# Optimization experiments

Hardware: AMD Instinct MI355X
Metric: run time of the kernel (lower is better)

## Reference

```python
import jax, jax.numpy as jnp
import numpy as np

B, D, H, W, Q = 16, 768, 64, 64, 128


def setup_inputs() -> dict:
    key = jax.random.key(0)
    ks = jax.random.split(key, 6)
    s = 0.02  # param init scale
    return {
        "visual_feat": jax.random.normal(ks[0], (B, D, H, W), jnp.float32),
        "text_feat": jax.random.normal(ks[1], (B, Q, D), jnp.float32),
        "Wq": jax.random.normal(ks[2], (D, D), jnp.float32) * s,
        "bq": jnp.zeros((D,), jnp.float32),
        "Wk": jax.random.normal(ks[3], (D, D), jnp.float32) * s,
        "bk": jnp.zeros((D,), jnp.float32),
        "Wv": jax.random.normal(ks[4], (D, D), jnp.float32) * s,
        "bv": jnp.zeros((D,), jnp.float32),
    }


def _entropy_weights(x):
    # x: [B, T, D] -> softmax over features, per-token entropy, softmax over tokens -> [B, T]
    p = jax.nn.softmax(x, axis=-1)
    ent = -jnp.sum(p * jnp.log(p + 1e-9), axis=-1)
    return jax.nn.softmax(ent, axis=-1)


def reference(visual_feat, text_feat, Wq, bq, Wk, bk, Wv, bv):
    b, d, h, w = visual_feat.shape
    vf = visual_feat.reshape(b, d, h * w).transpose(0, 2, 1)  # [B, N, D]
    ve = _entropy_weights(vf)          # [B, N]
    te = _entropy_weights(text_feat)   # [B, Q]
    q = vf @ Wq.T + bq                 # [B, N, D]
    k = text_feat @ Wk.T + bk          # [B, Q, D]
    v = text_feat @ Wv.T + bv          # [B, Q, D]
    attn = jnp.einsum('bnd,bqd->bnq', q, k) / jnp.sqrt(jnp.float32(d))
    attn = attn * (ve[:, :, None] * te[:, None, :])  # entropy outer-product modulation
    attn = jax.nn.softmax(attn, axis=-1)
    enhanced = jnp.einsum('bnq,bqd->bnd', attn, v)   # [B, N, D]
    return enhanced.transpose(0, 2, 1).reshape(b, d, h, w)
```

## Files before the change

kernel.cpp:

```cpp
#include <hip/hip_runtime.h>

#define B_ 16
#define D_ 768
#define N_ 4096
#define Q_ 128

typedef __attribute__((ext_vector_type(4))) float f32x4;
typedef __attribute__((ext_vector_type(8))) short short8;
typedef __attribute__((ext_vector_type(4))) short sv4;

__device__ __forceinline__ unsigned short f2bf(float f) {
  union { float f; unsigned u; } x; x.f = f;
  unsigned u = x.u;
  unsigned r = u + 0x7fffu + ((u >> 16) & 1u);
  return (unsigned short)(r >> 16);
}
__device__ __forceinline__ float bf2f(unsigned short h) {
  union { unsigned u; float f; } x; x.u = ((unsigned)h) << 16;
  return x.f;
}

__global__ __launch_bounds__(256) void prep_kernel(
    const float* __restrict__ Wk, const float* __restrict__ Wv,
    const float* __restrict__ Wq, const float* __restrict__ text,
    unsigned short* __restrict__ Wkb, unsigned short* __restrict__ Wvb,
    unsigned short* __restrict__ WqTb, unsigned short* __restrict__ textb,
    float* __restrict__ ent_t) {
  __shared__ float tile[32][33];
  const int z = blockIdx.z;
  const int t = threadIdx.x;
  if (z <= 1) {
    const float* src = z ? Wv : Wk;
    unsigned short* dst = z ? Wvb : Wkb;
    int i = (blockIdx.y * 24 + blockIdx.x) * 256 + t;
    float4 v = ((const float4*)src)[i];
    ushort4 o;
    o.x = f2bf(v.x); o.y = f2bf(v.y); o.z = f2bf(v.z); o.w = f2bf(v.w);
    ((ushort4*)dst)[i] = o;
  } else if (z == 2) {
    int bx = blockIdx.x * 32, by = blockIdx.y * 32;
    int tx = t & 31, ty = t >> 5;
    #pragma unroll
    for (int i = 0; i < 32; i += 8)
      tile[ty + i][tx] = Wq[(size_t)(by + ty + i) * D_ + bx + tx];
    __syncthreads();
    #pragma unroll
    for (int i = 0; i < 32; i += 8)
      WqTb[(size_t)(bx + ty + i) * D_ + by + tx] = f2bf(tile[tx][ty + i]);
  } else {
    int idx = blockIdx.y * 24 + blockIdx.x;
    if (idx >= 512) return;
    int row = idx * 4 + (t >> 6);
    int lane = t & 63;
    const float4* src = (const float4*)(text + (size_t)row * D_);
    ushort4* dst = (ushort4*)(textb + (size_t)row * D_);
    float s = 0.f, tt = 0.f;
    #pragma unroll
    for (int j = 0; j < 3; j++) {
      float4 v = src[lane + 64 * j];
      float e0 = __expf(v.x), e1 = __expf(v.y), e2 = __expf(v.z), e3 = __expf(v.w);
      s += (e0 + e1) + (e2 + e3);
      tt += v.x * e0 + v.y * e1;
      tt += v.z * e2 + v.w * e3;
      ushort4 o;
      o.x = f2bf(v.x); o.y = f2bf(v.y); o.z = f2bf(v.z); o.w = f2bf(v.w);
      dst[lane + 64 * j] = o;
    }
    #pragma unroll
    for (int off = 32; off; off >>= 1) {
      s += __shfl_xor(s, off);
      tt += __shfl_xor(tt, off);
    }
    if (lane == 0) ent_t[row] = __logf(s) - tt / s;
  }
}

__global__ __launch_bounds__(256) void gemm_kvT_kernel(
    const unsigned short* __restrict__ A, const unsigned short* __restrict__ Wkb,
    const float* __restrict__ bk, unsigned short* __restrict__ kb,
    const unsigned short* __restrict__ Wvb, const float* __restrict__ bv,
    unsigned short* __restrict__ vTb) {
  constexpr int LDA = 72;
  __shared__ unsigned short As[64 * LDA];
  __shared__ unsigned short Bs[64 * LDA];
  const bool isV = blockIdx.y >= 12;
  const unsigned short* Bm = isV ? Wvb : Wkb;
  const float* bias = isV ? bv : bk;
  unsigned short* C = isV ? vTb : kb;
  int m0 = blockIdx.x * 64, n0 = (isV ? blockIdx.y - 12 : blockIdx.y) * 64;
  int t = threadIdx.x, wave = t >> 6, lane = t & 63;
  int wm = (wave & 1) * 32, wn = (wave >> 1) * 32;
  int fl = lane & 15, fq = lane >> 4;
  f32x4 acc[2][2];
  #pragma unroll
  for (int i = 0; i < 2; i++)
    #pragma unroll
    for (int j = 0; j < 2; j++) acc[i][j] = {0.f, 0.f, 0.f, 0.f};
  for (int k0 = 0; k0 < D_; k0 += 64) {
    __syncthreads();
    #pragma unroll
    for (int i = 0; i < 2; i++) {
      int c = t + 256 * i;
      int sr = c >> 3, sc = (c & 7) * 8;
      *(uint4*)(As + sr * LDA + sc) = *(const uint4*)(A + (size_t)(m0 + sr) * D_ + k0 + sc);
      *(uint4*)(Bs + sr * LDA + sc) = *(const uint4*)(Bm + (size_t)(n0 + sr) * D_ + k0 + sc);
    }
    __syncthreads();
    #pragma unroll
    for (int ks = 0; ks < 2; ks++) {
      short8 afr[2], bfr[2];
      #pragma unroll
      for (int i = 0; i < 2; i++)
        afr[i] = *(const short8*)(As + (wm + i * 16 + fl) * LDA + ks * 32 + fq * 8);
      #pragma unroll
      for (int j = 0; j < 2; j++)
        bfr[j] = *(const short8*)(Bs + (wn + j * 16 + fl) * LDA + ks * 32 + fq * 8);
      #pragma unroll
      for (int i = 0; i < 2; i++)
        #pragma unroll
        for (int j = 0; j < 2; j++)
          acc[i][j] = __builtin_amdgcn_mfma_f32_16x16x32_bf16(afr[i], bfr[j], acc[i][j], 0, 0, 0);
    }
  }
  #pragma unroll
  for (int i = 0; i < 2; i++)
    #pragma unroll
    for (int j = 0; j < 2; j++) {
      int n = n0 + wn + j * 16 + fl;
      float bb = bias[n];
      #pragma unroll
      for (int r = 0; r < 4; r++) {
        int m = m0 + wm + i * 16 + fq * 4 + r;
        float val = acc[i][j][r] + bb;
        if (isV) {
          int bt = m >> 7, q = m & 127;
          C[((size_t)bt * D_ + n) * Q_ + q] = f2bf(val);
        } else {
          C[(size_t)m * D_ + n] = f2bf(val);
        }
      }
    }
}

__global__ __launch_bounds__(256) void gemm_kq_bias_kernel(
    const unsigned short* __restrict__ kb, const unsigned short* __restrict__ WqTb,
    unsigned short* __restrict__ kqb, const float* __restrict__ bq,
    float* __restrict__ skq) {
  constexpr int LDA = 72;
  __shared__ unsigned short As[64 * LDA];
  __shared__ unsigned short Bs[64 * LDA];
  const int t = threadIdx.x;
  if (blockIdx.y >= 12) {
    int idx = (blockIdx.y - 12) * 32 + blockIdx.x;
    int row = idx * 4 + (t >> 6);
    int lane = t & 63;
    const unsigned short* kr = kb + (size_t)row * D_;
    float s = 0.f;
    for (int k = lane; k < D_; k += 64) s += bq[k] * bf2f(kr[k]);
    #pragma unroll
    for (int off = 32; off; off >>= 1) s += __shfl_xor(s, off);
    if (lane == 0) skq[row] = s;
    return;
  }
  int m0 = blockIdx.x * 64, n0 = blockIdx.y * 64;
  int wave = t >> 6, lane = t & 63;
  int wm = (wave & 1) * 32, wn = (wave >> 1) * 32;
  int fl = lane & 15, fq = lane >> 4;
  f32x4 acc[2][2];
  #pragma unroll
  for (int i = 0; i < 2; i++)
    #pragma unroll
    for (int j = 0; j < 2; j++) acc[i][j] = {0.f, 0.f, 0.f, 0.f};
  for (int k0 = 0; k0 < D_; k0 += 64) {
    __syncthreads();
    #pragma unroll
    for (int i = 0; i < 2; i++) {
      int c = t + 256 * i;
      int sr = c >> 3, sc = (c & 7) * 8;
      *(uint4*)(As + sr * LDA + sc) = *(const uint4*)(kb + (size_t)(m0 + sr) * D_ + k0 + sc);
      *(uint4*)(Bs + sr * LDA + sc) = *(const uint4*)(WqTb + (size_t)(n0 + sr) * D_ + k0 + sc);
    }
    __syncthreads();
    #pragma unroll
    for (int ks = 0; ks < 2; ks++) {
      short8 afr[2], bfr[2];
      #pragma unroll
      for (int i = 0; i < 2; i++)
        afr[i] = *(const short8*)(As + (wm + i * 16 + fl) * LDA + ks * 32 + fq * 8);
      #pragma unroll
      for (int j = 0; j < 2; j++)
        bfr[j] = *(const short8*)(Bs + (wn + j * 16 + fl) * LDA + ks * 32 + fq * 8);
      #pragma unroll
      for (int i = 0; i < 2; i++)
        #pragma unroll
        for (int j = 0; j < 2; j++)
          acc[i][j] = __builtin_amdgcn_mfma_f32_16x16x32_bf16(afr[i], bfr[j], acc[i][j], 0, 0, 0);
    }
  }
  #pragma unroll
  for (int i = 0; i < 2; i++)
    #pragma unroll
    for (int j = 0; j < 2; j++) {
      int n = n0 + wn + j * 16 + fl;
      #pragma unroll
      for (int r = 0; r < 4; r++) {
        int m = m0 + wm + i * 16 + fq * 4 + r;
        kqb[(size_t)m * D_ + n] = f2bf(acc[i][j][r]);
      }
    }
}

__global__ __launch_bounds__(256, 2) void attn_s_kernel(
    const float* __restrict__ vis,
    const unsigned short* __restrict__ kq,
    float* __restrict__ S,
    float* __restrict__ ent_v)
{
  constexpr int LA = 68;
  constexpr int LB = 72;
  __shared__ unsigned short As[64 * LA];
  __shared__ unsigned short Bs[128 * LB];
  __shared__ float esh[512];

  const int bb = blockIdx.x >> 6;
  const int n0 = (blockIdx.x & 63) * 64;
  const int t = threadIdx.x;
  const int wave = t >> 6, lane = t & 63;
  const int fl = lane & 15, fq = lane >> 4;
  const int wm = (wave & 1) * 32;
  const int wq = (wave >> 1) * 64;

  const float* abase = vis + (size_t)bb * D_ * N_ + n0;
  const unsigned short* bbase = kq + (size_t)bb * Q_ * D_;

  f32x4 acc[2][4];
  #pragma unroll
  for (int i = 0; i < 2; i++)
    #pragma unroll
    for (int j = 0; j < 4; j++) acc[i][j] = {0.f, 0.f, 0.f, 0.f};

  const int smi = t & 63;
  const int ph = t >> 6;
  float es = 0.f, ets = 0.f;

  for (int k0 = 0; k0 < D_; k0 += 64) {
    __syncthreads();
    #pragma unroll
    for (int i = 0; i < 8; i++) {
      const int kk = 2 * (ph + 4 * i);
      const float v0 = abase[(size_t)(k0 + kk) * N_ + smi];
      const float v1 = abase[(size_t)(k0 + kk + 1) * N_ + smi];
      const float e0 = __expf(v0), e1 = __expf(v1);
      es += e0 + e1;
      ets += v0 * e0 + v1 * e1;
      const unsigned pk = (unsigned)f2bf(v0) | ((unsigned)f2bf(v1) << 16);
      *(unsigned*)(As + smi * LA + kk) = pk;
    }
    #pragma unroll
    for (int i = 0; i < 4; i++) {
      const int c = t + 256 * i;
      const int q = c >> 3, kc = (c & 7) * 8;
      const uint4 v = *(const uint4*)(bbase + (size_t)q * D_ + k0 + kc);
      *(uint4*)(Bs + q * LB + kc) = v;
    }
    __syncthreads();
    #pragma unroll
    for (int ks = 0; ks < 2; ks++) {
      short8 afr[2], bfr[4];
      #pragma unroll
      for (int i = 0; i < 2; i++) {
        const unsigned short* pa = As + (wm + i * 16 + fl) * LA + ks * 32 + fq * 8;
        sv4 lo = *(const sv4*)pa;
        sv4 hi = *(const sv4*)(pa + 4);
        afr[i] = __builtin_shufflevector(lo, hi, 0, 1, 2, 3, 4, 5, 6, 7);
      }
      #pragma unroll
      for (int j = 0; j < 4; j++)
        bfr[j] = *(const short8*)(Bs + (wq + j * 16 + fl) * LB + ks * 32 + fq * 8);
      #pragma unroll
      for (int i = 0; i < 2; i++)
        #pragma unroll
        for (int j = 0; j < 4; j++)
          acc[i][j] = __builtin_amdgcn_mfma_f32_16x16x32_bf16(afr[i], bfr[j], acc[i][j], 0, 0, 0);
    }
  }

  esh[t] = es;
  esh[256 + t] = ets;
  __syncthreads();
  if (t < 64) {
    const float Sx = esh[t] + esh[t + 64] + esh[t + 128] + esh[t + 192];
    const float Tx = esh[256 + t] + esh[320 + t] + esh[384 + t] + esh[448 + t];
    ent_v[(size_t)bb * N_ + n0 + t] = __logf(Sx) - Tx / Sx;
  }

  float* sbase = S + ((size_t)bb * N_ + n0) * Q_;
  #pragma unroll
  for (int i = 0; i < 2; i++)
    #pragma unroll
    for (int j = 0; j < 4; j++)
      #pragma unroll
      for (int r = 0; r < 4; r++)
        sbase[(size_t)(wm + i * 16 + fq * 4 + r) * Q_ + wq + j * 16 + fl] = acc[i][j][r];
}

__global__ __launch_bounds__(256, 2) void attn_pv_kernel(
    const float* __restrict__ S,
    const unsigned short* __restrict__ vT,
    const float* __restrict__ ent_v,
    const float* __restrict__ ent_t,
    const float* __restrict__ skq,
    float* __restrict__ out)
{
  constexpr int LP = 136;
  __shared__ unsigned short Ps[64 * LP];
  __shared__ unsigned short Vs[64 * LP];
  __shared__ float stats[2][64][2];
  __shared__ float tesh[128];
  __shared__ float vesh[64];
  __shared__ float zred[4];
  __shared__ float zsum, tsum;

  const int bb = blockIdx.x >> 6;
  const int n0 = (blockIdx.x & 63) * 64;
  const int t = threadIdx.x;
  const int wave = t >> 6, lane = t & 63;
  const int fl = lane & 15, fq = lane >> 4;
  const int wm = (wave & 1) * 32;
  const int wq = (wave >> 1) * 64;

  const float* evb = ent_v + (size_t)bb * N_;
  float zp = 0.f;
  #pragma unroll
  for (int i = 0; i < 16; i++) zp += __expf(evb[t + 256 * i]);
  #pragma unroll
  for (int off = 32; off; off >>= 1) zp += __shfl_xor(zp, off);
  if (lane == 0) zred[wave] = zp;
  if (t < 128) tesh[t] = __expf(ent_t[bb * 128 + t]);
  if (t < 64) vesh[t] = __expf(evb[n0 + t]);
  __syncthreads();
  if (t == 0) zsum = zred[0] + zred[1] + zred[2] + zred[3];
  if (t < 64) {
    float s = tesh[t] + tesh[t + 64];
    #pragma unroll
    for (int off = 32; off; off >>= 1) s += __shfl_xor(s, off);
    if (t == 0) tsum = s;
  }
  __syncthreads();
  const float rZ = 1.0f / zsum;
  const float rT = 1.0f / tsum;

  f32x4 acc[2][4];
  const float* sbase = S + ((size_t)bb * N_ + n0) * Q_;
  #pragma unroll
  for (int i = 0; i < 2; i++)
    #pragma unroll
    for (int j = 0; j < 4; j++)
      #pragma unroll
      for (int r = 0; r < 4; r++)
        acc[i][j][r] = sbase[(size_t)(wm + i * 16 + fq * 4 + r) * Q_ + wq + j * 16 + fl];

  const float rsD = 0.03608439182435161f;
  float tev[4], skv[4];
  #pragma unroll
  for (int j = 0; j < 4; j++) {
    int q = wq + j * 16 + fl;
    tev[j] = tesh[q] * rT;
    skv[j] = skq[bb * Q_ + q];
  }
  float vev4[2][4];
  #pragma unroll
  for (int i = 0; i < 2; i++)
    #pragma unroll
    for (int r = 0; r < 4; r++)
      vev4[i][r] = vesh[wm + i * 16 + fq * 4 + r] * rZ;

  float rmax[2][4], rsum[2][4];
  #pragma unroll
  for (int i = 0; i < 2; i++)
    #pragma unroll
    for (int r = 0; r < 4; r++) rmax[i][r] = -__builtin_inff();
  #pragma unroll
  for (int i = 0; i < 2; i++)
    #pragma unroll
    for (int j = 0; j < 4; j++)
      #pragma unroll
      for (int r = 0; r < 4; r++) {
        float L = (acc[i][j][r] + skv[j]) * rsD * vev4[i][r] * tev[j];
        acc[i][j][r] = L;
        rmax[i][r] = fmaxf(rmax[i][r], L);
      }
  #pragma unroll
  for (int off = 1; off < 16; off <<= 1)
    #pragma unroll
    for (int i = 0; i < 2; i++)
      #pragma unroll
      for (int r = 0; r < 4; r++)
        rmax[i][r] = fmaxf(rmax[i][r], __shfl_xor(rmax[i][r], off));
  #pragma unroll
  for (int i = 0; i < 2; i++)
    #pragma unroll
    for (int r = 0; r < 4; r++) rsum[i][r] = 0.f;
  #pragma unroll
  for (int i = 0; i < 2; i++)
    #pragma unroll
    for (int j = 0; j < 4; j++)
      #pragma unroll
      for (int r = 0; r < 4; r++) {
        float e = __expf(acc[i][j][r] - rmax[i][r]);
        acc[i][j][r] = e;
        rsum[i][r] += e;
      }
  #pragma unroll
  for (int off = 1; off < 16; off <<= 1)
    #pragma unroll
    for (int i = 0; i < 2; i++)
      #pragma unroll
      for (int r = 0; r < 4; r++) rsum[i][r] += __shfl_xor(rsum[i][r], off);

  const int qh = wq >> 6;
  if (fl == 0) {
    #pragma unroll
    for (int i = 0; i < 2; i++)
      #pragma unroll
      for (int r = 0; r < 4; r++) {
        int m = wm + i * 16 + fq * 4 + r;
        stats[qh][m][0] = rmax[i][r];
        stats[qh][m][1] = rsum[i][r];
      }
  }
  __syncthreads();
  float fac[2][4];
  #pragma unroll
  for (int i = 0; i < 2; i++)
    #pragma unroll
    for (int r = 0; r < 4; r++) {
      int m = wm + i * 16 + fq * 4 + r;
      float M2 = stats[1 - qh][m][0], S2 = stats[1 - qh][m][1];
      float Mf = fmaxf(rmax[i][r], M2);
      float sf = rsum[i][r] * __expf(rmax[i][r] - Mf) + S2 * __expf(M2 - Mf);
      fac[i][r] = __expf(rmax[i][r] - Mf) / sf;
    }
  #pragma unroll
  for (int i = 0; i < 2; i++)
    #pragma unroll
    for (int j = 0; j < 4; j++)
      #pragma unroll
      for (int r = 0; r < 4; r++) {
        int m = wm + i * 16 + fq * 4 + r;
        int q = wq + j * 16 + fl;
        Ps[m * LP + q] = f2bf(acc[i][j][r] * fac[i][r]);
      }

  const int wd = (wave & 1) * 32;
  const int wm2 = (wave >> 1) * 32;
  for (int dc = 0; dc < 12; dc++) {
    __syncthreads();
    const unsigned short* vbase = vT + ((size_t)bb * D_ + dc * 64) * Q_;
    #pragma unroll
    for (int i = 0; i < 4; i++) {
      const int c = t + 256 * i;
      const int d = c >> 4, qc = (c & 15) * 8;
      *(uint4*)(Vs + d * LP + qc) = *(const uint4*)(vbase + (size_t)d * Q_ + qc);
    }
    __syncthreads();
    f32x4 acc2[2][2];
    #pragma unroll
    for (int i = 0; i < 2; i++)
      #pragma unroll
      for (int j = 0; j < 2; j++) acc2[i][j] = {0.f, 0.f, 0.f, 0.f};
    #pragma unroll
    for (int ks = 0; ks < 4; ks++) {
      short8 vfr[2], pfr[2];
      #pragma unroll
      for (int i = 0; i < 2; i++)
        vfr[i] = *(const short8*)(Vs + (wd + i * 16 + fl) * LP + ks * 32 + fq * 8);
      #pragma unroll
      for (int j = 0; j < 2; j++)
        pfr[j] = *(const short8*)(Ps + (wm2 + j * 16 + fl) * LP + ks * 32 + fq * 8);
      #pragma unroll
      for (int i = 0; i < 2; i++)
        #pragma unroll
        for (int j = 0; j < 2; j++)
          acc2[i][j] = __builtin_amdgcn_mfma_f32_16x16x32_bf16(vfr[i], pfr[j], acc2[i][j], 0, 0, 0);
    }
    float* obase = out + ((size_t)bb * D_ + dc * 64) * N_ + n0;
    #pragma unroll
    for (int i = 0; i < 2; i++)
      #pragma unroll
      for (int j = 0; j < 2; j++) {
        int mm = wm2 + j * 16 + fl;
        #pragma unroll
        for (int r = 0; r < 4; r++) {
          int d = wd + i * 16 + fq * 4 + r;
          obase[(size_t)d * N_ + mm] = acc2[i][j][r];
        }
      }
  }
}

extern "C" void kernel_launch(void* const* d_in, const int* in_sizes, int n_in,
                              void* d_out, int out_size, void* d_ws, size_t ws_size,
                              hipStream_t stream) {
  const float* vis  = (const float*)d_in[0];
  const float* text = (const float*)d_in[1];
  const float* Wq   = (const float*)d_in[2];
  const float* bq   = (const float*)d_in[3];
  const float* Wk   = (const float*)d_in[4];
  const float* bk   = (const float*)d_in[5];
  const float* Wv   = (const float*)d_in[6];
  const float* bv   = (const float*)d_in[7];
  float* out = (float*)d_out;
  char* ws = (char*)d_ws;

  unsigned short* textb = (unsigned short*)(ws + 0);
  unsigned short* Wkb   = (unsigned short*)(ws + 3145728);
  unsigned short* Wvb   = (unsigned short*)(ws + 4325376);
  unsigned short* WqTb  = (unsigned short*)(ws + 5505024);
  unsigned short* kb    = (unsigned short*)(ws + 6684672);
  unsigned short* kqb   = (unsigned short*)(ws + 9830400);
  unsigned short* vTb   = (unsigned short*)(ws + 12976128);
  float* ent_t = (float*)(ws + 16121856);
  float* ent_v = (float*)(ws + 16138240);
  float* skq   = (float*)(ws + 16662528);
  float* Sbuf  = (float*)(ws + 16777216);

  prep_kernel<<<dim3(24, 24, 4), 256, 0, stream>>>(Wk, Wv, Wq, text,
                                                   Wkb, Wvb, WqTb, textb, ent_t);
  gemm_kvT_kernel<<<dim3(32, 24), 256, 0, stream>>>(textb, Wkb, bk, kb, Wvb, bv, vTb);
  gemm_kq_bias_kernel<<<dim3(32, 28), 256, 0, stream>>>(kb, WqTb, kqb, bq, skq);
  attn_s_kernel<<<1024, 256, 0, stream>>>(vis, kqb, Sbuf, ent_v);
  attn_pv_kernel<<<1024, 256, 0, stream>>>(Sbuf, vTb, ent_v, ent_t, skq, out);
}
```

Baseline: 430.7 us.

## Vectorize visual loads, store S in fragment layout, stage output through LDS

Measured after the change: 437.9 us. No clear change (+1.7%).

```diff
diff --git a/kernel.cpp b/kernel.cpp
--- a/kernel.cpp
+++ b/kernel.cpp
@@ -239,22 +239,23 @@
     #pragma unroll
     for (int j = 0; j < 4; j++) acc[i][j] = {0.f, 0.f, 0.f, 0.f};
 
-  const int smi = t & 63;
-  const int ph = t >> 6;
-  float es = 0.f, ets = 0.f;
+  const int col4 = t & 15;
+  float es4[4] = {0.f, 0.f, 0.f, 0.f}, ets4[4] = {0.f, 0.f, 0.f, 0.f};
 
   for (int k0 = 0; k0 < D_; k0 += 64) {
     __syncthreads();
     #pragma unroll
-    for (int i = 0; i < 8; i++) {
-      const int kk = 2 * (ph + 4 * i);
-      const float v0 = abase[(size_t)(k0 + kk) * N_ + smi];
-      const float v1 = abase[(size_t)(k0 + kk + 1) * N_ + smi];
-      const float e0 = __expf(v0), e1 = __expf(v1);
-      es += e0 + e1;
-      ets += v0 * e0 + v1 * e1;
-      const unsigned pk = (unsigned)f2bf(v0) | ((unsigned)f2bf(v1) << 16);
-      *(unsigned*)(As + smi * LA + kk) = pk;
+    for (int i = 0; i < 4; i++) {
+      const int row = (t >> 4) + 16 * i;
+      const float4 v = *(const float4*)(abase + (size_t)(k0 + row) * N_ + col4 * 4);
+      const float vv[4] = {v.x, v.y, v.z, v.w};
+      #pragma unroll
+      for (int j = 0; j < 4; j++) {
+        const float e = __expf(vv[j]);
+        es4[j] += e;
+        ets4[j] += vv[j] * e;
+        As[(col4 * 4 + j) * LA + row] = f2bf(vv[j]);
+      }
     }
     #pragma unroll
     for (int i = 0; i < 4; i++) {
@@ -285,23 +286,33 @@
     }
   }
 
-  esh[t] = es;
-  esh[256 + t] = ets;
+  #pragma unroll
+  for (int j = 0; j < 4; j++) {
+    es4[j] += __shfl_xor(es4[j], 16);
+    es4[j] += __shfl_xor(es4[j], 32);
+    ets4[j] += __shfl_xor(ets4[j], 16);
+    ets4[j] += __shfl_xor(ets4[j], 32);
+  }
+  if (lane < 16) {
+    #pragma unroll
+    for (int j = 0; j < 4; j++) {
+      esh[wave * 64 + lane * 4 + j] = es4[j];
+      esh[256 + wave * 64 + lane * 4 + j] = ets4[j];
+    }
+  }
   __syncthreads();
   if (t < 64) {
-    const float Sx = esh[t] + esh[t + 64] + esh[t + 128] + esh[t + 192];
+    const float Sx = esh[t] + esh[64 + t] + esh[128 + t] + esh[192 + t];
     const float Tx = esh[256 + t] + esh[320 + t] + esh[384 + t] + esh[448 + t];
     ent_v[(size_t)bb * N_ + n0 + t] = __logf(Sx) - Tx / Sx;
   }
 
-  float* sbase = S + ((size_t)bb * N_ + n0) * Q_;
+  float* sfrag = S + ((size_t)blockIdx.x * 256 + t) * 32;
   #pragma unroll
   for (int i = 0; i < 2; i++)
     #pragma unroll
     for (int j = 0; j < 4; j++)
-      #pragma unroll
-      for (int r = 0; r < 4; r++)
-        sbase[(size_t)(wm + i * 16 + fq * 4 + r) * Q_ + wq + j * 16 + fl] = acc[i][j][r];
+      *(f32x4*)(sfrag + (i * 4 + j) * 4) = acc[i][j];
 }
 
 __global__ __launch_bounds__(256, 2) void attn_pv_kernel(
@@ -313,6 +324,7 @@
     float* __restrict__ out)
 {
   constexpr int LP = 136;
+  constexpr int LN = 68;
   __shared__ unsigned short Ps[64 * LP];
   __shared__ unsigned short Vs[64 * LP];
   __shared__ float stats[2][64][2];
@@ -320,6 +332,7 @@
   __shared__ float vesh[64];
   __shared__ float zred[4];
   __shared__ float zsum, tsum;
+  float* Os = (float*)Vs;
 
   const int bb = blockIdx.x >> 6;
   const int n0 = (blockIdx.x & 63) * 64;
@@ -351,14 +364,12 @@
   const float rT = 1.0f / tsum;
 
   f32x4 acc[2][4];
-  const float* sbase = S + ((size_t)bb * N_ + n0) * Q_;
+  const float* sfrag = S + ((size_t)blockIdx.x * 256 + t) * 32;
   #pragma unroll
   for (int i = 0; i < 2; i++)
     #pragma unroll
     for (int j = 0; j < 4; j++)
-      #pragma unroll
-      for (int r = 0; r < 4; r++)
-        acc[i][j][r] = sbase[(size_t)(wm + i * 16 + fq * 4 + r) * Q_ + wq + j * 16 + fl];
+      acc[i][j] = *(const f32x4*)(sfrag + (i * 4 + j) * 4);
 
   const float rsD = 0.03608439182435161f;
   float tev[4], skv[4];
@@ -484,7 +495,7 @@
         for (int j = 0; j < 2; j++)
           acc2[i][j] = __builtin_amdgcn_mfma_f32_16x16x32_bf16(vfr[i], pfr[j], acc2[i][j], 0, 0, 0);
     }
-    float* obase = out + ((size_t)bb * D_ + dc * 64) * N_ + n0;
+    __syncthreads();
     #pragma unroll
     for (int i = 0; i < 2; i++)
       #pragma unroll
@@ -493,9 +504,17 @@
         #pragma unroll
         for (int r = 0; r < 4; r++) {
           int d = wd + i * 16 + fq * 4 + r;
-          obase[(size_t)d * N_ + mm] = acc2[i][j][r];
+          Os[d * LN + mm] = acc2[i][j][r];
         }
       }
+    __syncthreads();
+    float* obase = out + ((size_t)bb * D_ + dc * 64) * N_ + n0;
+    #pragma unroll
+    for (int i = 0; i < 4; i++) {
+      const int c = t + 256 * i;
+      const int d = c >> 4, cg = c & 15;
+      *(float4*)(obase + (size_t)d * N_ + cg * 4) = *(const float4*)(Os + d * LN + cg * 4);
+    }
   }
 }
 
```
